# Kernel tuning notes

Measured on AMD Instinct MI355X. Metric: run time of the kernel, lower is better.

## Reference

```python
import jax, jax.numpy as jnp
import numpy as np

VAR = (0.1, 0.2)          # encode variances (SSD convention used in MutualGuide)
F_ALPHA, F_GAMMA = 0.25, 1.0   # FocalLoss(alpha=0.25, gamma=1.0)
L_ALPHA, L_GAMMA, L_BETA = 0.5, 1.5, 0.11  # BalancedL1Loss

def point_form(p):
    # [P,4] cxcywh -> xyxy
    return jnp.concatenate([p[:, :2] - p[:, 2:] / 2, p[:, :2] + p[:, 2:] / 2], axis=1)

def jaccard(a, b):
    # a: [T,4] xyxy truths, b: [P,4] xyxy priors -> IoU [T,P]
    lt = jnp.maximum(a[:, None, :2], b[None, :, :2])
    rb = jnp.minimum(a[:, None, 2:], b[None, :, 2:])
    wh = jnp.clip(rb - lt, 0.0)
    inter = wh[..., 0] * wh[..., 1]
    area_a = ((a[:, 2] - a[:, 0]) * (a[:, 3] - a[:, 1]))[:, None]
    area_b = ((b[:, 2] - b[:, 0]) * (b[:, 3] - b[:, 1]))[None, :]
    return inter / (area_a + area_b - inter)

def match_one(truths, labels, priors_pt):
    # truths [T,4], labels [T] int, priors_pt [P,4]
    T = truths.shape[0]
    ov = jaccard(truths, priors_pt)                 # [T,P]
    best_truth_ov = ov.max(axis=0)                  # [P]
    best_truth_idx = ov.argmax(axis=0)              # [P]
    best_prior_idx = ov.argmax(axis=1)              # [T]
    # force each gt's best prior to be positive (index_fill_ with 2)
    best_truth_ov = best_truth_ov.at[best_prior_idx].set(2.0)
    best_truth_idx = best_truth_idx.at[best_prior_idx].set(jnp.arange(T))
    matches = truths[best_truth_idx]                # [P,4] xyxy
    conf = labels[best_truth_idx] + 1               # [P], 0 reserved for bg
    return matches, conf, best_truth_ov

def encode(matched, priors):
    # matched xyxy [N,4], priors cxcywh [N.,4]
    g_cxcy = ((matched[..., :2] + matched[..., 2:]) / 2 - priors[..., :2]) / (VAR[0] * priors[..., 2:])
    g_wh = jnp.log((matched[..., 2:] - matched[..., :2]) / priors[..., 2:]) / VAR[1]
    return jnp.concatenate([g_cxcy, g_wh], axis=-1)

def balanced_l1(pred, target):
    b = np.exp(L_GAMMA / L_ALPHA) - 1.0
    d = jnp.abs(pred - target)
    small = L_ALPHA / b * (b * d + 1.0) * jnp.log(b * d / L_BETA + 1.0) - L_ALPHA * d
    large = L_GAMMA * d + L_GAMMA / b - L_ALPHA * L_BETA
    return jnp.where(d < L_BETA, small, large)

def sigmoid_focal(logits, t):
    p = jax.nn.sigmoid(logits)
    ce = -(t * jax.nn.log_sigmoid(logits) + (1.0 - t) * jax.nn.log_sigmoid(-logits))
    pt = t * (1.0 - p) + (1.0 - t) * p
    w = (F_ALPHA * t + (1.0 - F_ALPHA) * (1.0 - t)) * pt ** F_GAMMA
    return w * ce

def setup_inputs() -> dict:
    key = jax.random.key(0)
    kl, kc, kp1, kp2, kt1, kt2, ktl = jax.random.split(key, 7)
    B, P, C, T = 16, 16384, 80, 32
    loc_data = jax.random.normal(kl, (B, P, 4), jnp.float32) * 0.1
    conf_data = jax.random.normal(kc, (B, P, C), jnp.float32)
    p_cxcy = jax.random.uniform(kp1, (P, 2), jnp.float32, 0.05, 0.95)
    p_wh = jax.random.uniform(kp2, (P, 2), jnp.float32, 0.02, 0.3)
    priors = jnp.concatenate([p_cxcy, p_wh], axis=1)
    t_c = jax.random.uniform(kt1, (B, T, 2), jnp.float32, 0.2, 0.8)
    t_wh = jax.random.uniform(kt2, (B, T, 2), jnp.float32, 0.05, 0.3)
    boxes = jnp.concatenate([jnp.clip(t_c - t_wh / 2, 0.0, 1.0), jnp.clip(t_c + t_wh / 2, 0.0, 1.0)], axis=-1)
    labels = jax.random.randint(ktl, (B, T), 0, C).astype(jnp.float32)
    targets = jnp.concatenate([boxes, labels[..., None]], axis=-1)  # [B,T,5]
    return {"loc_data": loc_data, "conf_data": conf_data, "priors": priors, "targets": targets}

def reference(loc_data, conf_data, priors, targets):
    B, P, C = conf_data.shape
    truths = targets[..., :4]
    labels = targets[..., 4].astype(jnp.int32)
    priors_pt = point_form(priors)
    loc_t, conf_t, overlap_t = jax.vmap(match_one, in_axes=(0, 0, None))(truths, labels, priors_pt)
    # masks (non-mutual-guide path)
    pos = overlap_t >= 0.5                                  # [B,P]
    ign = (overlap_t < 0.5) & (overlap_t >= 0.4)
    neg = overlap_t < 0.4
    # localization loss over positives (mean over masked elements)
    loc_targets = encode(loc_t, priors[None, :, :])          # [B,P,4]
    l1 = balanced_l1(loc_data, loc_targets)                  # [B,P,4]
    n_pos = jnp.maximum(pos.sum(), 1)
    loss_l = (l1 * pos[..., None]).sum() / (4.0 * n_pos)
    # classification: one-hot minus background, flip ignored rows to -1
    conf_t = jnp.where(neg, 0, conf_t)
    onehot = jax.nn.one_hot(conf_t, C + 1, dtype=conf_data.dtype)[..., 1:]  # [B,P,C]
    batch_label = jnp.where(ign[..., None], -onehot, onehot)
    mask = batch_label >= 0
    t = jnp.where(mask, batch_label, 0.0)
    fl = sigmoid_focal(conf_data, t)
    loss_c = (fl * mask).sum() / jnp.maximum(mask.sum(), 1)
    return (loss_l, loss_c)
```

## Files before the change

kernel.cpp:

```cpp
#include <hip/hip_runtime.h>

#pragma clang fp contract(off)

#define B_SZ 16
#define P_SZ 16384
#define C_SZ 80
#define T_SZ 32
#define NCHUNK 32

struct PartialL { float l; float pad; unsigned pos; unsigned ign; };

__device__ __forceinline__ float iou_ref(float ax0, float ay0, float ax1, float ay1, float aarea,
                                         float bx0, float by0, float bx1, float by1, float barea) {
    float lx = fmaxf(ax0, bx0), ly = fmaxf(ay0, by0);
    float rx = fminf(ax1, bx1), ry = fminf(ay1, by1);
    float w = fmaxf(rx - lx, 0.0f), h = fmaxf(ry - ly, 0.0f);
    float inter = w * h;
    float denom = (aarea + barea) - inter;
    return inter / denom;
}

__global__ __launch_bounds__(256) void match_kernel(const float* __restrict__ priors,
                                                    const float* __restrict__ targets,
                                                    unsigned long long* __restrict__ keys) {
    const int b = blockIdx.y;
    const int p0 = blockIdx.x * 512;
    const int tid = threadIdx.x;

    __shared__ float tx0[T_SZ], ty0[T_SZ], tx1[T_SZ], ty1[T_SZ], tar[T_SZ];
    __shared__ float red_ov[4][T_SZ];
    __shared__ int   red_ix[4][T_SZ];

    if (tid < T_SZ) {
        const float* tp = targets + (b * T_SZ + tid) * 5;
        float x0 = tp[0], y0 = tp[1], x1 = tp[2], y1 = tp[3];
        tx0[tid] = x0; ty0[tid] = y0; tx1[tid] = x1; ty1[tid] = y1;
        tar[tid] = (x1 - x0) * (y1 - y0);
    }
    __syncthreads();

    float bov[T_SZ];
    int   bpi[T_SZ];
#pragma unroll
    for (int t = 0; t < T_SZ; ++t) { bov[t] = -1.0f; bpi[t] = 0x7FFFFFFF; }

#pragma unroll
    for (int i = 0; i < 2; ++i) {
        int p = p0 + tid + i * 256;
        float4 pr = reinterpret_cast<const float4*>(priors)[p];
        float px0 = pr.x - pr.z * 0.5f, py0 = pr.y - pr.w * 0.5f;
        float px1 = pr.x + pr.z * 0.5f, py1 = pr.y + pr.w * 0.5f;
        float parea = (px1 - px0) * (py1 - py0);
#pragma unroll
        for (int t = 0; t < T_SZ; ++t) {
            float iou = iou_ref(tx0[t], ty0[t], tx1[t], ty1[t], tar[t], px0, py0, px1, py1, parea);
            if (iou > bov[t]) { bov[t] = iou; bpi[t] = p; }
        }
    }

    const int lane = tid & 63, wid = tid >> 6;
#pragma unroll
    for (int t = 0; t < T_SZ; ++t) {
        float v = bov[t]; int ix = bpi[t];
#pragma unroll
        for (int off = 32; off > 0; off >>= 1) {
            float v2 = __shfl_down(v, off, 64);
            int   i2 = __shfl_down(ix, off, 64);
            if (v2 > v || (v2 == v && i2 < ix)) { v = v2; ix = i2; }
        }
        if (lane == 0) { red_ov[wid][t] = v; red_ix[wid][t] = ix; }
    }
    __syncthreads();

    if (tid < T_SZ) {
        float v = red_ov[0][tid]; int ix = red_ix[0][tid];
#pragma unroll
        for (int w = 1; w < 4; ++w) {
            float v2 = red_ov[w][tid]; int i2 = red_ix[w][tid];
            if (v2 > v || (v2 == v && i2 < ix)) { v = v2; ix = i2; }
        }
        unsigned long long key = (((unsigned long long)__float_as_uint(v)) << 32)
                               | (unsigned long long)(0xFFFFFFFFu - (unsigned)ix);
        keys[(b * NCHUNK + blockIdx.x) * T_SZ + tid] = key;
    }
}

__device__ __forceinline__ float bl1(float pred, float target) {
    const float bC   = (float)19.085536923187668;
    const float aob  = (float)(0.5 / 19.085536923187668);
    const float cL   = (float)(1.5 / 19.085536923187668 - 0.055);
    float d = fabsf(pred - target);
    if (d < 0.11f) {
        return aob * (bC * d + 1.0f) * __logf(bC * d / 0.11f + 1.0f) - 0.5f * d;
    }
    return 1.5f * d + cL;
}

__device__ __forceinline__ float focal(float x, bool isT) {
    float u  = __expf(-fabsf(x));
    float L  = __logf(1.0f + u);
    float q  = __builtin_amdgcn_rcpf(1.0f + u);
    float p  = (x >= 0.0f) ? q : 1.0f - q;
    float xp = fmaxf(x, 0.0f);
    float xn = xp - x;
    return isT ? 0.25f * (1.0f - p) * (xn + L) : 0.75f * p * (xp + L);
}

__global__ __launch_bounds__(256) void flags_kernel(const float* __restrict__ loc_data,
                                                    const float* __restrict__ priors,
                                                    const float* __restrict__ targets,
                                                    const unsigned long long* __restrict__ keys,
                                                    unsigned short* __restrict__ codes,
                                                    PartialL* __restrict__ pl_out) {
    const int b = blockIdx.y;
    const int p0 = blockIdx.x * 256;
    const int tid = threadIdx.x;
    const int p = p0 + tid;

    __shared__ float tx0[T_SZ], ty0[T_SZ], tx1[T_SZ], ty1[T_SZ], tar[T_SZ];
    __shared__ int tlab[T_SZ], bp[T_SZ];
    __shared__ float rf[4];
    __shared__ int rp[4], ri[4];

    if (tid < T_SZ) {
        const float* tp = targets + (b * T_SZ + tid) * 5;
        float x0 = tp[0], y0 = tp[1], x1 = tp[2], y1 = tp[3];
        tx0[tid] = x0; ty0[tid] = y0; tx1[tid] = x1; ty1[tid] = y1;
        tar[tid] = (x1 - x0) * (y1 - y0);
        tlab[tid] = (int)tp[4];
        const unsigned long long* kb = keys + b * (NCHUNK * T_SZ) + tid;
        unsigned long long k = kb[0];
#pragma unroll
        for (int w = 1; w < NCHUNK; ++w) {
            unsigned long long k2 = kb[w * T_SZ];
            if (k2 > k) k = k2;
        }
        bp[tid] = (int)(0xFFFFFFFFu - (unsigned)(k & 0xFFFFFFFFull));
    }
    __syncthreads();

    float4 pr = reinterpret_cast<const float4*>(priors)[p];
    float px0 = pr.x - pr.z * 0.5f, py0 = pr.y - pr.w * 0.5f;
    float px1 = pr.x + pr.z * 0.5f, py1 = pr.y + pr.w * 0.5f;
    float parea = (px1 - px0) * (py1 - py0);

    float ov = -1.0f; int idx = 0;
#pragma unroll
    for (int t = 0; t < T_SZ; ++t) {
        float iou = iou_ref(tx0[t], ty0[t], tx1[t], ty1[t], tar[t], px0, py0, px1, py1, parea);
        if (iou > ov) { ov = iou; idx = t; }
    }
#pragma unroll
    for (int t = 0; t < T_SZ; ++t) if (bp[t] == p) { ov = 2.0f; idx = t; }

    int fl = (ov >= 0.5f) ? 1 : ((ov >= 0.4f) ? 2 : 0);
    int tc = tlab[idx];
    codes[b * P_SZ + p] = (unsigned short)((tc << 2) | fl);

    float sum_l = 0.0f;
    int pos_c = 0, ign_c = 0;
    if (fl == 1) {
        pos_c = 1;
        float4 ld = reinterpret_cast<const float4*>(loc_data)[b * P_SZ + p];
        float mx0 = tx0[idx], my0 = ty0[idx], mx1 = tx1[idx], my1 = ty1[idx];
        float gx = ((mx0 + mx1) * 0.5f - pr.x) / (0.1f * pr.z);
        float gy = ((my0 + my1) * 0.5f - pr.y) / (0.1f * pr.w);
        float gw = __logf((mx1 - mx0) / pr.z) / 0.2f;
        float gh = __logf((my1 - my0) / pr.w) / 0.2f;
        sum_l = bl1(ld.x, gx) + bl1(ld.y, gy) + bl1(ld.z, gw) + bl1(ld.w, gh);
    } else if (fl == 2) {
        ign_c = 1;
    }

    const int lane = tid & 63, wid = tid >> 6;
#pragma unroll
    for (int off = 32; off > 0; off >>= 1) {
        sum_l += __shfl_down(sum_l, off, 64);
        pos_c += __shfl_down(pos_c, off, 64);
        ign_c += __shfl_down(ign_c, off, 64);
    }
    if (lane == 0) { rf[wid] = sum_l; rp[wid] = pos_c; ri[wid] = ign_c; }
    __syncthreads();
    if (tid == 0) {
        PartialL o;
        o.l = rf[0] + rf[1] + rf[2] + rf[3];
        o.pad = 0.0f;
        o.pos = (unsigned)(rp[0] + rp[1] + rp[2] + rp[3]);
        o.ign = (unsigned)(ri[0] + ri[1] + ri[2] + ri[3]);
        pl_out[b * 64 + blockIdx.x] = o;
    }
}

__global__ __launch_bounds__(256) void conf_kernel(const float* __restrict__ conf_data,
                                                   const unsigned short* __restrict__ codes,
                                                   float* __restrict__ pc_out) {
    const int b = blockIdx.y;
    const int p0 = blockIdx.x * 128;
    const int tid = threadIdx.x;

    const float4* cbase = reinterpret_cast<const float4*>(conf_data + ((size_t)(b * P_SZ + p0)) * C_SZ);
    const unsigned short* cdb = codes + b * P_SZ + p0;

    float4 v[10];
    unsigned short cd[10];
#pragma unroll
    for (int it = 0; it < 10; ++it) {
        int j = tid + it * 256;
        v[it] = cbase[j];
        cd[it] = cdb[j / 20];
    }

    float sum_c = 0.0f;
#pragma unroll
    for (int it = 0; it < 10; ++it) {
        int j = tid + it * 256;
        int pl = j / 20;
        int c0 = (j - pl * 20) * 4;
        int f = cd[it] & 3;
        int g = (cd[it] >> 2) - c0;
        float s = 0.0f;
        {
            float fk = focal(v[it].x, (f == 1) && (g == 0));
            if (!((f == 2) && (g == 0))) s += fk;
        }
        {
            float fk = focal(v[it].y, (f == 1) && (g == 1));
            if (!((f == 2) && (g == 1))) s += fk;
        }
        {
            float fk = focal(v[it].z, (f == 1) && (g == 2));
            if (!((f == 2) && (g == 2))) s += fk;
        }
        {
            float fk = focal(v[it].w, (f == 1) && (g == 3));
            if (!((f == 2) && (g == 3))) s += fk;
        }
        sum_c += s;
    }

    __shared__ float rf[4];
    const int lane = tid & 63, wid = tid >> 6;
#pragma unroll
    for (int off = 32; off > 0; off >>= 1) sum_c += __shfl_down(sum_c, off, 64);
    if (lane == 0) rf[wid] = sum_c;
    __syncthreads();
    if (tid == 0) pc_out[b * 128 + blockIdx.x] = rf[0] + rf[1] + rf[2] + rf[3];
}

__global__ __launch_bounds__(256) void finalize_kernel(const PartialL* __restrict__ pl,
                                                       const float* __restrict__ pc,
                                                       float* __restrict__ out) {
    const int tid = threadIdx.x;
    __shared__ double r_l[4], r_c[4];
    __shared__ unsigned long long r_p[4], r_i[4];

    double sl = 0.0, sc = 0.0;
    unsigned long long np = 0, ni = 0;
#pragma unroll
    for (int k = 0; k < 4; ++k) {
        PartialL p = pl[tid + k * 256];
        sl += (double)p.l; np += p.pos; ni += p.ign;
    }
#pragma unroll
    for (int k = 0; k < 8; ++k) sc += (double)pc[tid + k * 256];

    const int lane = tid & 63, wid = tid >> 6;
#pragma unroll
    for (int off = 32; off > 0; off >>= 1) {
        sl += __shfl_down(sl, off, 64);
        sc += __shfl_down(sc, off, 64);
        np += __shfl_down(np, off, 64);
        ni += __shfl_down(ni, off, 64);
    }
    if (lane == 0) { r_l[wid] = sl; r_c[wid] = sc; r_p[wid] = np; r_i[wid] = ni; }
    __syncthreads();
    if (tid == 0) {
        double tl = r_l[0] + r_l[1] + r_l[2] + r_l[3];
        double tc = r_c[0] + r_c[1] + r_c[2] + r_c[3];
        unsigned long long tp = r_p[0] + r_p[1] + r_p[2] + r_p[3];
        long long ti = (long long)(r_i[0] + r_i[1] + r_i[2] + r_i[3]);
        double npos = (tp < 1ull) ? 1.0 : (double)tp;
        long long msum = (long long)B_SZ * P_SZ * C_SZ - ti;
        if (msum < 1) msum = 1;
        out[0] = (float)(tl / (4.0 * npos));
        out[1] = (float)(tc / (double)msum);
    }
}

extern "C" void kernel_launch(void* const* d_in, const int* in_sizes, int n_in,
                              void* d_out, int out_size, void* d_ws, size_t ws_size,
                              hipStream_t stream) {
    const float* loc     = (const float*)d_in[0];
    const float* conf    = (const float*)d_in[1];
    const float* priors  = (const float*)d_in[2];
    const float* targets = (const float*)d_in[3];

    char* ws = (char*)d_ws;
    unsigned long long* keys = (unsigned long long*)ws;
    unsigned short*    codes = (unsigned short*)(ws + 131072);
    PartialL*          plp   = (PartialL*)(ws + 655360);
    float*             pcp   = (float*)(ws + 671744);

    match_kernel<<<dim3(NCHUNK, 16), 256, 0, stream>>>(priors, targets, keys);
    flags_kernel<<<dim3(64, 16), 256, 0, stream>>>(loc, priors, targets, keys, codes, plp);
    conf_kernel<<<dim3(128, 16), 256, 0, stream>>>(conf, codes, pcp);
    finalize_kernel<<<1, 256, 0, stream>>>(plp, pcp, (float*)d_out);
}
```

Baseline: 65.48 us.

## Fuse finalize into conf kernel via last-block ticket and simplify focal math

Removes the separate finalize launch by having the last conf block, found through an atomic ticket that match_kernel resets, perform the final reduction. The focal loss is rewritten as a single scaled sigmoid-times-softplus expression with a sign flip, which drops a branch and some arithmetic. Loads are split into two halves of five float4 each, and launch bounds now request 8 blocks per CU to raise occupancy. In exchange there is an atomic and threadfence per block, plus a dependency on correct ticket reset ordering across kernels.

```diff
diff --git a/kernel.cpp b/kernel.cpp
--- a/kernel.cpp
+++ b/kernel.cpp
@@ -22,10 +22,13 @@
 
 __global__ __launch_bounds__(256) void match_kernel(const float* __restrict__ priors,
                                                     const float* __restrict__ targets,
-                                                    unsigned long long* __restrict__ keys) {
+                                                    unsigned long long* __restrict__ keys,
+                                                    unsigned* __restrict__ ticket) {
     const int b = blockIdx.y;
     const int p0 = blockIdx.x * 512;
     const int tid = threadIdx.x;
+
+    if (blockIdx.x == 0 && blockIdx.y == 0 && tid == 0) *ticket = 0;
 
     __shared__ float tx0[T_SZ], ty0[T_SZ], tx1[T_SZ], ty1[T_SZ], tar[T_SZ];
     __shared__ float red_ov[4][T_SZ];
@@ -94,16 +97,6 @@
         return aob * (bC * d + 1.0f) * __logf(bC * d / 0.11f + 1.0f) - 0.5f * d;
     }
     return 1.5f * d + cL;
-}
-
-__device__ __forceinline__ float focal(float x, bool isT) {
-    float u  = __expf(-fabsf(x));
-    float L  = __logf(1.0f + u);
-    float q  = __builtin_amdgcn_rcpf(1.0f + u);
-    float p  = (x >= 0.0f) ? q : 1.0f - q;
-    float xp = fmaxf(x, 0.0f);
-    float xn = xp - x;
-    return isT ? 0.25f * (1.0f - p) * (xn + L) : 0.75f * p * (xp + L);
 }
 
 __global__ __launch_bounds__(256) void flags_kernel(const float* __restrict__ loc_data,
@@ -191,9 +184,24 @@
     }
 }
 
-__global__ __launch_bounds__(256) void conf_kernel(const float* __restrict__ conf_data,
-                                                   const unsigned short* __restrict__ codes,
-                                                   float* __restrict__ pc_out) {
+__device__ __forceinline__ float focal1(float x, float scale, bool flip) {
+    float a = fabsf(x);
+    float e = __expf(-a);
+    float d = 1.0f + e;
+    float r = __builtin_amdgcn_rcpf(d);
+    float L = __logf(d);
+    float y = flip ? -x : x;
+    float sig = (y >= 0.0f) ? r : e * r;
+    float sp  = fmaxf(y, 0.0f) + L;
+    return scale * (sig * sp);
+}
+
+__global__ __launch_bounds__(256, 8) void conf_kernel(const float* __restrict__ conf_data,
+                                                      const unsigned short* __restrict__ codes,
+                                                      const PartialL* __restrict__ pl,
+                                                      float* __restrict__ pc_out,
+                                                      unsigned* __restrict__ ticket,
+                                                      float* __restrict__ out) {
     const int b = blockIdx.y;
     const int p0 = blockIdx.x * 128;
     const int tid = threadIdx.x;
@@ -201,41 +209,36 @@
     const float4* cbase = reinterpret_cast<const float4*>(conf_data + ((size_t)(b * P_SZ + p0)) * C_SZ);
     const unsigned short* cdb = codes + b * P_SZ + p0;
 
-    float4 v[10];
-    unsigned short cd[10];
-#pragma unroll
-    for (int it = 0; it < 10; ++it) {
-        int j = tid + it * 256;
-        v[it] = cbase[j];
-        cd[it] = cdb[j / 20];
-    }
-
     float sum_c = 0.0f;
 #pragma unroll
-    for (int it = 0; it < 10; ++it) {
-        int j = tid + it * 256;
-        int pl = j / 20;
-        int c0 = (j - pl * 20) * 4;
-        int f = cd[it] & 3;
-        int g = (cd[it] >> 2) - c0;
-        float s = 0.0f;
-        {
-            float fk = focal(v[it].x, (f == 1) && (g == 0));
-            if (!((f == 2) && (g == 0))) s += fk;
-        }
-        {
-            float fk = focal(v[it].y, (f == 1) && (g == 1));
-            if (!((f == 2) && (g == 1))) s += fk;
-        }
-        {
-            float fk = focal(v[it].z, (f == 1) && (g == 2));
-            if (!((f == 2) && (g == 2))) s += fk;
-        }
-        {
-            float fk = focal(v[it].w, (f == 1) && (g == 3));
-            if (!((f == 2) && (g == 3))) s += fk;
-        }
-        sum_c += s;
+    for (int half = 0; half < 2; ++half) {
+        float4 v[5];
+        unsigned short cd[5];
+#pragma unroll
+        for (int i = 0; i < 5; ++i) {
+            int j = tid + (half * 5 + i) * 256;
+            v[i] = cbase[j];
+            cd[i] = cdb[j / 20];
+        }
+#pragma unroll
+        for (int i = 0; i < 5; ++i) {
+            int j = tid + (half * 5 + i) * 256;
+            int pl_ = j / 20;
+            int c0 = (j - pl_ * 20) * 4;
+            int f = cd[i] & 3;
+            int g = (cd[i] >> 2) - c0;
+            float xs0 = v[i].x, xs1 = v[i].y, xs2 = v[i].z, xs3 = v[i].w;
+            bool m0 = (g == 0), m1 = (g == 1), m2 = (g == 2), m3 = (g == 3);
+            bool pos = (f == 1), ign = (f == 2);
+            float s0 = (ign && m0) ? 0.0f : ((pos && m0) ? 0.25f : 0.75f);
+            float s1 = (ign && m1) ? 0.0f : ((pos && m1) ? 0.25f : 0.75f);
+            float s2 = (ign && m2) ? 0.0f : ((pos && m2) ? 0.25f : 0.75f);
+            float s3 = (ign && m3) ? 0.0f : ((pos && m3) ? 0.25f : 0.75f);
+            sum_c += focal1(xs0, s0, pos && m0);
+            sum_c += focal1(xs1, s1, pos && m1);
+            sum_c += focal1(xs2, s2, pos && m2);
+            sum_c += focal1(xs3, s3, pos && m3);
+        }
     }
 
     __shared__ float rf[4];
@@ -244,27 +247,29 @@
     for (int off = 32; off > 0; off >>= 1) sum_c += __shfl_down(sum_c, off, 64);
     if (lane == 0) rf[wid] = sum_c;
     __syncthreads();
-    if (tid == 0) pc_out[b * 128 + blockIdx.x] = rf[0] + rf[1] + rf[2] + rf[3];
-}
-
-__global__ __launch_bounds__(256) void finalize_kernel(const PartialL* __restrict__ pl,
-                                                       const float* __restrict__ pc,
-                                                       float* __restrict__ out) {
-    const int tid = threadIdx.x;
+    __shared__ bool is_last;
+    if (tid == 0) {
+        pc_out[b * 128 + blockIdx.x] = rf[0] + rf[1] + rf[2] + rf[3];
+        __threadfence();
+        unsigned old = atomicAdd(ticket, 1u);
+        is_last = (old == 2047u);
+    }
+    __syncthreads();
+    if (!is_last) return;
+    __threadfence();
+
+    double sl = 0.0, sc = 0.0;
+    unsigned long long np = 0, ni = 0;
+#pragma unroll
+    for (int k = 0; k < 4; ++k) {
+        PartialL q = pl[tid + k * 256];
+        sl += (double)q.l; np += q.pos; ni += q.ign;
+    }
+#pragma unroll
+    for (int k = 0; k < 8; ++k) sc += (double)pc_out[tid + k * 256];
+
     __shared__ double r_l[4], r_c[4];
     __shared__ unsigned long long r_p[4], r_i[4];
-
-    double sl = 0.0, sc = 0.0;
-    unsigned long long np = 0, ni = 0;
-#pragma unroll
-    for (int k = 0; k < 4; ++k) {
-        PartialL p = pl[tid + k * 256];
-        sl += (double)p.l; np += p.pos; ni += p.ign;
-    }
-#pragma unroll
-    for (int k = 0; k < 8; ++k) sc += (double)pc[tid + k * 256];
-
-    const int lane = tid & 63, wid = tid >> 6;
 #pragma unroll
     for (int off = 32; off > 0; off >>= 1) {
         sl += __shfl_down(sl, off, 64);
@@ -300,9 +305,9 @@
     unsigned short*    codes = (unsigned short*)(ws + 131072);
     PartialL*          plp   = (PartialL*)(ws + 655360);
     float*             pcp   = (float*)(ws + 671744);
-
-    match_kernel<<<dim3(NCHUNK, 16), 256, 0, stream>>>(priors, targets, keys);
+    unsigned*          tick  = (unsigned*)(ws + 679936);
+
+    match_kernel<<<dim3(NCHUNK, 16), 256, 0, stream>>>(priors, targets, keys, tick);
     flags_kernel<<<dim3(64, 16), 256, 0, stream>>>(loc, priors, targets, keys, codes, plp);
-    conf_kernel<<<dim3(128, 16), 256, 0, stream>>>(conf, codes, pcp);
-    finalize_kernel<<<1, 256, 0, stream>>>(plp, pcp, (float*)d_out);
-}
+    conf_kernel<<<dim3(128, 16), 256, 0, stream>>>(conf, codes, plp, pcp, tick, (float*)d_out);
+}
```

Result: slower. 115.1 us (+75.8%).
